# Performance work log

Hardware: AMD Instinct MI355X
Metric: run time of the kernel (lower is better)

## Reference

```python
import jax, jax.numpy as jnp
import numpy as np

L, T, D = 3, 65536, 256


def setup_inputs() -> dict:
    key = jax.random.key(0)
    ks = jax.random.split(key, 10)
    stdv = 1.0 / np.sqrt(D)
    u = lambda k, shape: jax.random.uniform(k, shape, jnp.float32, -stdv, stdv)
    return {
        "story": jax.random.normal(ks[0], (T, D), jnp.float32),
        "question": jax.random.normal(ks[1], (D,), jnp.float32),
        "Wz_f": u(ks[2], (L, D, D)),
        "bz_f": u(ks[3], (L, D)),
        "Wh_f": u(ks[4], (L, 2 * D, D)),
        "bh_f": u(ks[5], (L, D)),
        "Wz_b": u(ks[6], (L, D, D)),
        "bz_b": u(ks[7], (L, D)),
        "Wh_b": u(ks[8], (L, 2 * D, D)),
        "bh_b": u(ks[9], (L, D)),
    }


def _qrn_dir(x, q, Wz, bz, Wh, bh):
    """One QRN layer in one direction. x, q: [T, D]. Returns h states [T, D]."""
    z = jax.nn.sigmoid((x * q) @ Wz + bz)                      # [T, D]
    h_tilde = jnp.tanh(jnp.concatenate([x, q], axis=-1) @ Wh + bh)  # [T, D]
    a = 1.0 - z            # multiplicative factor on h_prev
    b = z * h_tilde        # additive term
    # linear recurrence h_t = a_t * h_{t-1} + b_t, h_0 = 0 -> associative scan
    def comb(c1, c2):
        a1, b1 = c1
        a2, b2 = c2
        return a1 * a2, a2 * b1 + b2
    _, h = jax.lax.associative_scan(comb, (a, b), axis=0)
    return h  # h[t] = hidden state after statement t


def reference(story, question, Wz_f, bz_f, Wh_f, bh_f, Wz_b, bz_b, Wh_b, bh_b):
    q = jnp.broadcast_to(question, story.shape)  # layer-0 question per step
    for layer in range(L):
        h_fwd = _qrn_dir(story, q, Wz_f[layer], bz_f[layer], Wh_f[layer], bh_f[layer])
        # backward direction: reversed story with correspondingly reversed questions
        h_bwd_rev = _qrn_dir(story[::-1], q[::-1], Wz_b[layer], bz_b[layer],
                             Wh_b[layer], bh_b[layer])
        if layer < L - 1:
            # q_{t}^{k+1} = h_fwd_t + h_bwd_t (aligned back to forward order)
            q = h_fwd + h_bwd_rev[::-1]
    return h_fwd[-1]  # final forward hidden state of last layer, [D]
```

## Files before the change

kernel.cpp:

```cpp
#include <hip/hip_runtime.h>
#include <hip/hip_bf16.h>
#include <math.h>

#define D    256
#define BT   128
#define GN   128
#define BN   64
#define NSEG 32

typedef unsigned short u16;
typedef unsigned int   u32;
typedef __attribute__((ext_vector_type(8))) short short8;
typedef __attribute__((ext_vector_type(4))) float floatx4;

__device__ __forceinline__ float b2f(u16 v) {
    union { unsigned u; float f; } x; x.u = ((unsigned)v) << 16; return x.f;
}
__device__ __forceinline__ u16 f2b(float f) {
    union { unsigned u; float f; } x; x.f = f;
    unsigned lsb = (x.u >> 16) & 1;
    x.u += 0x7fffu + lsb;
    return (u16)(x.u >> 16);
}
__device__ __forceinline__ float sigm(float x) {
    return __builtin_amdgcn_rcpf(1.0f + __expf(-x));
}
__device__ __forceinline__ float tanhfast(float x) {
    return 1.0f - 2.0f * __builtin_amdgcn_rcpf(__expf(2.0f * x) + 1.0f);
}
__device__ __forceinline__ void async16(const u16* g, u16* l) {
    __builtin_amdgcn_global_load_lds(
        (const __attribute__((address_space(1))) unsigned int*)g,
        (__attribute__((address_space(3))) unsigned int*)l, 16, 0, 0);
}

__global__ __launch_bounds__(256) void wtrans_kernel(
    const float* __restrict__ Wz_f, const float* __restrict__ Wh_f,
    const float* __restrict__ Wz_b, const float* __restrict__ Wh_b,
    u16* __restrict__ wt)
{
    int id = blockIdx.x * 256 + threadIdx.x;
    int combo = id / (3 * 65536);
    int rem   = id % (3 * 65536);
    int m = rem >> 16;
    int e = rem & 65535;
    int k = e >> 8, n = e & 255;
    int l   = combo < 3 ? combo : combo - 3;
    int dir = combo < 3 ? 0 : 1;
    float v;
    if (m == 0) {
        const float* Wz = dir ? Wz_b : Wz_f;
        v = Wz[((size_t)l * D + k) * D + n];
    } else {
        const float* Wh = dir ? Wh_b : Wh_f;
        int kk = (m == 2) ? (k + D) : k;
        v = Wh[((size_t)l * 2 * D + kk) * D + n];
    }
    wt[(size_t)combo * 3 * 65536 + (size_t)m * 65536 + (size_t)n * D + k] = f2b(v);
}

__global__ __launch_bounds__(256) void prep0_kernel(
    const float* __restrict__ story, const float* __restrict__ question,
    u16* __restrict__ xb, u16* __restrict__ q, u16* __restrict__ xq)
{
    long id = (long)blockIdx.x * 256 + threadIdx.x;
    long row = id >> 5;
    int  d0  = (int)(id & 31) * 8;
    const float* xp = story + row * D + d0;
    float4 xa = *(const float4*)xp;
    float4 xc = *(const float4*)(xp + 4);
    float xv[8] = {xa.x, xa.y, xa.z, xa.w, xc.x, xc.y, xc.z, xc.w};
    short8 xs, qs, xqs;
    #pragma unroll
    for (int i = 0; i < 8; ++i) {
        u16 qb = f2b(question[d0 + i]);
        xs[i]  = (short)f2b(xv[i]);
        qs[i]  = (short)qb;
        xqs[i] = (short)f2b(xv[i] * b2f(qb));
    }
    long o = id * 8;
    *(short8*)(xb + o) = xs;
    *(short8*)(q  + o) = qs;
    *(short8*)(xq + o) = xqs;
}

struct StageS {
    u16 ax [BT * 32]; u16 aq [BT * 32]; u16 axq[BT * 32];
    u16 bz_[GN * 32]; u16 bx_[GN * 32]; u16 bq_[GN * 32];
};
struct EpiP { float segA[NSEG][GN]; float segB[NSEG][GN]; };
union __align__(16) SharedP { StageS st; EpiP ep; };

__device__ __forceinline__ void gemm_body(
    SharedP& sh, int tid, int c, int n0,
    const u16* xbg, const u16* qg, const u16* xqg, const u16* wt,
    const float* bz, const float* bh,
    float* aggA, float* aggB, u32* abg, int FWD)
{
    const int t0   = c * BT;
    const int lane = tid & 63, w = tid >> 6;
    const int wr = w & 1, wc = w >> 1;
    const int lr   = lane & 15, quad = lane >> 4;

    const int swA   = (quad ^ ((lr >> 1) & 3)) * 8;
    const int offA0 = (wr * 64 + lr) * 32 + swA;
    const int offB0 = (wc * 32 + lr) * 32 + swA;

    floatx4 accz[4][2], acch[4][2];
    #pragma unroll
    for (int rt = 0; rt < 4; ++rt)
        #pragma unroll
        for (int ct = 0; ct < 2; ++ct) {
            accz[rt][ct] = (floatx4){0.f,0.f,0.f,0.f};
            acch[rt][ct] = (floatx4){0.f,0.f,0.f,0.f};
        }

    const int lb = (tid & ~63) * 8;

    const int arow = tid >> 2;
    const int agg_ = (tid & 3) ^ ((arow >> 1) & 3);
    const size_t goA = (size_t)(t0 + arow) * D + agg_ * 8;
    const size_t goB = (size_t)(n0 + arow) * D + agg_ * 8;
    const u16* pax  = xbg + goA;
    const u16* paq  = qg  + goA;
    const u16* paxq = xqg + goA;
    const u16* pbz  = wt + goB;
    const u16* pbx  = wt + 65536  + goB;
    const u16* pbq  = wt + 131072 + goB;

    #pragma unroll
    for (int k0 = 0; k0 < D; k0 += 32) {
        async16(pax  + k0, sh.st.ax  + lb);
        async16(paq  + k0, sh.st.aq  + lb);
        async16(paxq + k0, sh.st.axq + lb);
        async16(pbz  + k0, sh.st.bz_ + lb);
        async16(pbx  + k0, sh.st.bx_ + lb);
        async16(pbq  + k0, sh.st.bq_ + lb);
        __syncthreads();

        short8 vz[2], vx[2], vq[2];
        #pragma unroll
        for (int ct = 0; ct < 2; ++ct) {
            vz[ct] = *(const short8*)(sh.st.bz_ + offB0 + ct * 512);
            vx[ct] = *(const short8*)(sh.st.bx_ + offB0 + ct * 512);
            vq[ct] = *(const short8*)(sh.st.bq_ + offB0 + ct * 512);
        }
        #pragma unroll
        for (int rt = 0; rt < 4; ++rt) {
            short8 fxq = *(const short8*)(sh.st.axq + offA0 + rt * 512);
            short8 fx  = *(const short8*)(sh.st.ax  + offA0 + rt * 512);
            short8 fq  = *(const short8*)(sh.st.aq  + offA0 + rt * 512);
            #pragma unroll
            for (int ct = 0; ct < 2; ++ct) {
                accz[rt][ct] = __builtin_amdgcn_mfma_f32_16x16x32_bf16(fxq, vz[ct], accz[rt][ct], 0, 0, 0);
                acch[rt][ct] = __builtin_amdgcn_mfma_f32_16x16x32_bf16(fx , vx[ct], acch[rt][ct], 0, 0, 0);
                acch[rt][ct] = __builtin_amdgcn_mfma_f32_16x16x32_bf16(fq , vq[ct], acch[rt][ct], 0, 0, 0);
            }
        }
        __syncthreads();
    }

    float bzn[2], bhn[2];
    #pragma unroll
    for (int ct = 0; ct < 2; ++ct) {
        int n = n0 + wc * 32 + ct * 16 + lr;
        bzn[ct] = bz[n]; bhn[ct] = bh[n];
    }
    #pragma unroll
    for (int rt = 0; rt < 4; ++rt) {
        #pragma unroll
        for (int ct = 0; ct < 2; ++ct) {
            float av[4], bvv[4];
            #pragma unroll
            for (int r = 0; r < 4; ++r) {
                float z  = sigm(accz[rt][ct][r] + bzn[ct]);
                float ht = tanhfast(acch[rt][ct][r] + bhn[ct]);
                av[r]  = 1.0f - z;
                bvv[r] = z * ht;
            }
            float A = 1.f, B = 0.f;
            if (FWD) {
                #pragma unroll
                for (int r = 0; r < 4; ++r) { A = av[r] * A; B = fmaf(av[r], B, bvv[r]); }
            } else {
                #pragma unroll
                for (int r = 3; r >= 0; --r) { A = av[r] * A; B = fmaf(av[r], B, bvv[r]); }
            }
            int seg = wr * 16 + rt * 4 + quad;
            int col = wc * 32 + ct * 16 + lr;
            sh.ep.segA[seg][col] = A;
            sh.ep.segB[seg][col] = B;
            if (abg) {
                size_t base = (size_t)(t0 + wr * 64 + rt * 16 + quad * 4) * D + n0 + col;
                #pragma unroll
                for (int r = 0; r < 4; ++r) {
                    u32 pv = (u32)f2b(av[r]) | ((u32)f2b(bvv[r]) << 16);
                    abg[base + (size_t)r * D] = pv;
                }
            }
        }
    }
    __syncthreads();

    if (tid < GN) {
        float A = 1.f, B = 0.f;
        if (FWD) {
            #pragma unroll
            for (int sg = 0; sg < NSEG; ++sg) {
                float a = sh.ep.segA[sg][tid];
                A = a * A; B = fmaf(a, B, sh.ep.segB[sg][tid]);
            }
        } else {
            #pragma unroll
            for (int sg = NSEG - 1; sg >= 0; --sg) {
                float a = sh.ep.segA[sg][tid];
                A = a * A; B = fmaf(a, B, sh.ep.segB[sg][tid]);
            }
        }
        aggA[(size_t)c * D + n0 + tid] = A;
        aggB[(size_t)c * D + n0 + tid] = B;
    }
}

template<int FWD, int ABOUT>
__global__ __launch_bounds__(512, 4) void qrn_g5(
    const u16* __restrict__ xbg, const u16* __restrict__ qg,
    const u16* __restrict__ xqg, const u16* __restrict__ wt,
    const float* __restrict__ bz, const float* __restrict__ bh,
    float* __restrict__ aggA, float* __restrict__ aggB,
    u32* __restrict__ abg)
{
    __shared__ SharedP sh;
    const int tid  = threadIdx.x;
    const int bid  = (int)blockIdx.x;
    const int gidx = (bid & 7) * 128 + (bid >> 3);
    gemm_body(sh, tid, gidx >> 1, (gidx & 1) * GN,
              xbg, qg, xqg, wt, bz, bh, aggA, aggB, ABOUT ? abg : nullptr, FWD);
}

__global__ __launch_bounds__(512, 4) void qrn_gboth(
    const u16* __restrict__ xbg, const u16* __restrict__ qg,
    const u16* __restrict__ xqg,
    const u16* __restrict__ wtF, const u16* __restrict__ wtB,
    const float* __restrict__ bzf, const float* __restrict__ bhf,
    const float* __restrict__ bzb, const float* __restrict__ bhb,
    float* __restrict__ aggAf, float* __restrict__ aggBf,
    float* __restrict__ aggAb, float* __restrict__ aggBb,
    u32* __restrict__ abf, u32* __restrict__ abb)
{
    __shared__ SharedP sh;
    const int tid  = threadIdx.x;
    const int half = (int)blockIdx.x >> 10;
    const int bid  = (int)blockIdx.x & 1023;
    const int gidx = (bid & 7) * 128 + (bid >> 3);
    gemm_body(sh, tid, gidx >> 1, (gidx & 1) * GN,
              xbg, qg, xqg,
              half ? wtB : wtF,
              half ? bzb : bzf, half ? bhb : bhf,
              half ? aggAb : aggAf, half ? aggBb : aggBf,
              half ? abb : abf, half ? 0 : 1);
}

__global__ __launch_bounds__(256) void replay_fb(
    const u32* __restrict__ abf, const u32* __restrict__ abb,
    const float* __restrict__ hinif, const float* __restrict__ hinib,
    const u16* __restrict__ xb, u16* __restrict__ qout, u16* __restrict__ xq)
{
    __shared__ u32   sab[BT * BN];
    __shared__ u16   hf16[BT * BN];
    __shared__ float sA[4][BN], sB[4][BN], hs[4][BN];
    const int tid = threadIdx.x;
    const int c   = (int)(blockIdx.x >> 2);
    const int n0  = ((int)blockIdx.x & 3) * BN;
    const int t0  = c * BT;
    const int sg = tid >> 6, n = tid & 63;

    #pragma unroll
    for (int i = 0; i < 8; ++i) {
        int idx = i * 256 + tid;
        int row = idx >> 4, g = idx & 15;
        *(uint4*)(sab + row * BN + g * 4) =
            *(const uint4*)(abf + (size_t)(t0 + row) * D + n0 + g * 4);
    }
    __syncthreads();
    {
        float A = 1.f, B = 0.f;
        #pragma unroll
        for (int i = 0; i < 32; ++i) {
            u32 v = sab[(sg * 32 + i) * BN + n];
            float a = b2f((u16)(v & 0xffff)), b = b2f((u16)(v >> 16));
            A = a * A; B = fmaf(a, B, b);
        }
        sA[sg][n] = A; sB[sg][n] = B;
    }
    __syncthreads();
    if (tid < BN) {
        float h = hinif[(size_t)c * D + n0 + tid];
        #pragma unroll
        for (int s = 0; s < 4; ++s) {
            hs[s][tid] = h;
            h = fmaf(sA[s][tid], h, sB[s][tid]);
        }
    }
    __syncthreads();
    {
        float h = hs[sg][n];
        #pragma unroll
        for (int i = 0; i < 32; ++i) {
            int t = sg * 32 + i;
            u32 v = sab[t * BN + n];
            float a = b2f((u16)(v & 0xffff)), b = b2f((u16)(v >> 16));
            h = fmaf(a, h, b);
            hf16[t * BN + n] = f2b(h);
        }
    }
    __syncthreads();

    #pragma unroll
    for (int i = 0; i < 8; ++i) {
        int idx = i * 256 + tid;
        int row = idx >> 4, g = idx & 15;
        *(uint4*)(sab + row * BN + g * 4) =
            *(const uint4*)(abb + (size_t)(t0 + row) * D + n0 + g * 4);
    }
    __syncthreads();
    {
        float A = 1.f, B = 0.f;
        #pragma unroll
        for (int i = 31; i >= 0; --i) {
            u32 v = sab[(sg * 32 + i) * BN + n];
            float a = b2f((u16)(v & 0xffff)), b = b2f((u16)(v >> 16));
            A = a * A; B = fmaf(a, B, b);
        }
        sA[sg][n] = A; sB[sg][n] = B;
    }
    __syncthreads();
    if (tid < BN) {
        float h = hinib[(size_t)c * D + n0 + tid];
        for (int s = 3; s >= 0; --s) {
            hs[s][tid] = h;
            h = fmaf(sA[s][tid], h, sB[s][tid]);
        }
    }
    __syncthreads();
    {
        float h = hs[sg][n];
        #pragma unroll
        for (int i = 31; i >= 0; --i) {
            int t = sg * 32 + i;
            u32 v = sab[t * BN + n];
            float a = b2f((u16)(v & 0xffff)), b = b2f((u16)(v >> 16));
            h = fmaf(a, h, b);
            size_t o = (size_t)(t0 + t) * D + n0 + n;
            float qn = b2f(hf16[t * BN + n]) + h;
            u16 qb = f2b(qn);
            qout[o] = qb;
            xq[o]   = f2b(b2f(xb[o]) * b2f(qb));
        }
    }
}

__global__ __launch_bounds__(256) void replay_f(
    const u32* __restrict__ abg, const float* __restrict__ hini,
    u16* __restrict__ qout)
{
    __shared__ u32   sab[BT * BN];
    __shared__ float sA[4][BN], sB[4][BN], hs[4][BN];
    const int tid = threadIdx.x;
    const int c   = (int)(blockIdx.x >> 2);
    const int n0  = ((int)blockIdx.x & 3) * BN;
    const int t0  = c * BT;

    #pragma unroll
    for (int i = 0; i < 8; ++i) {
        int idx = i * 256 + tid;
        int row = idx >> 4, g = idx & 15;
        *(uint4*)(sab + row * BN + g * 4) =
            *(const uint4*)(abg + (size_t)(t0 + row) * D + n0 + g * 4);
    }
    __syncthreads();

    const int sg = tid >> 6, n = tid & 63;
    float A = 1.f, B = 0.f;
    #pragma unroll
    for (int i = 0; i < 32; ++i) {
        u32 v = sab[(sg * 32 + i) * BN + n];
        float a = b2f((u16)(v & 0xffff)), b = b2f((u16)(v >> 16));
        A = a * A; B = fmaf(a, B, b);
    }
    sA[sg][n] = A; sB[sg][n] = B;
    __syncthreads();
    if (tid < BN) {
        float h = hini[(size_t)c * D + n0 + tid];
        #pragma unroll
        for (int s = 0; s < 4; ++s) {
            hs[s][tid] = h;
            h = fmaf(sA[s][tid], h, sB[s][tid]);
        }
    }
    __syncthreads();
    float h = hs[sg][n];
    #pragma unroll
    for (int i = 0; i < 32; ++i) {
        int t = sg * 32 + i;
        u32 v = sab[t * BN + n];
        float a = b2f((u16)(v & 0xffff)), b = b2f((u16)(v >> 16));
        h = fmaf(a, h, b);
        qout[(size_t)(t0 + t) * D + n0 + n] = f2b(h);
    }
}

__global__ __launch_bounds__(256) void replay_b(
    const u32* __restrict__ abg, const float* __restrict__ hini,
    const u16* __restrict__ xb, u16* __restrict__ qout, u16* __restrict__ xq)
{
    __shared__ u32   sab[BT * BN];
    __shared__ float sA[4][BN], sB[4][BN], hs[4][BN];
    const int tid = threadIdx.x;
    const int c   = (int)(blockIdx.x >> 2);
    const int n0  = ((int)blockIdx.x & 3) * BN;
    const int t0  = c * BT;

    #pragma unroll
    for (int i = 0; i < 8; ++i) {
        int idx = i * 256 + tid;
        int row = idx >> 4, g = idx & 15;
        *(uint4*)(sab + row * BN + g * 4) =
            *(const uint4*)(abg + (size_t)(t0 + row) * D + n0 + g * 4);
    }
    __syncthreads();

    const int sg = tid >> 6, n = tid & 63;
    float A = 1.f, B = 0.f;
    #pragma unroll
    for (int i = 31; i >= 0; --i) {
        u32 v = sab[(sg * 32 + i) * BN + n];
        float a = b2f((u16)(v & 0xffff)), b = b2f((u16)(v >> 16));
        A = a * A; B = fmaf(a, B, b);
    }
    sA[sg][n] = A; sB[sg][n] = B;
    __syncthreads();
    if (tid < BN) {
        float h = hini[(size_t)c * D + n0 + tid];
        for (int s = 3; s >= 0; --s) {
            hs[s][tid] = h;
            h = fmaf(sA[s][tid], h, sB[s][tid]);
        }
    }
    __syncthreads();
    float h = hs[sg][n];
    #pragma unroll
    for (int i = 31; i >= 0; --i) {
        int t = sg * 32 + i;
        u32 v = sab[t * BN + n];
        float a = b2f((u16)(v & 0xffff)), b = b2f((u16)(v >> 16));
        h = fmaf(a, h, b);
        size_t o = (size_t)(t0 + t) * D + n0 + n;
        float qn = b2f(qout[o]) + h;
        u16 qb = f2b(qn);
        qout[o] = qb;
        xq[o]   = f2b(b2f(xb[o]) * b2f(qb));
    }
}

__device__ __forceinline__ void scan_body(
    const float* aggA, const float* aggB, float* hinit, float* out_final,
    int fwd, int nch, int n, int tid)
{
    __shared__ float sA[256], sB[256];
    const int per = nch >> 8;
    float lA[4], lB[4];
    float A = 1.f, B = 0.f;
    for (int j = 0; j < per; ++j) {
        int pidx = tid * per + j;
        int c = fwd ? pidx : (nch - 1 - pidx);
        float a = aggA[(size_t)c * D + n];
        float b = aggB[(size_t)c * D + n];
        lA[j] = a; lB[j] = b;
        A = a * A;
        B = fmaf(a, B, b);
    }
    sA[tid] = A; sB[tid] = B;
    __syncthreads();
    for (int off = 1; off < 256; off <<= 1) {
        float pA = 1.f, pB = 0.f;
        if (tid >= off) { pA = sA[tid - off]; pB = sB[tid - off]; }
        __syncthreads();
        if (tid >= off) {
            float cA = sA[tid], cB = sB[tid];
            sA[tid] = pA * cA;
            sB[tid] = fmaf(cA, pB, cB);
        }
        __syncthreads();
    }
    float eB = (tid > 0) ? sB[tid - 1] : 0.f;
    for (int j = 0; j < per; ++j) {
        int pidx = tid * per + j;
        int c = fwd ? pidx : (nch - 1 - pidx);
        hinit[(size_t)c * D + n] = eB;
        eB = fmaf(lA[j], eB, lB[j]);
    }
    if (out_final != nullptr && tid == 0) out_final[n] = sB[255];
}

__global__ __launch_bounds__(256) void scan_p2_kernel(
    const float* __restrict__ aggA, const float* __restrict__ aggB,
    float* __restrict__ hinit, float* __restrict__ out_final, int fwd, int nch)
{
    scan_body(aggA, aggB, hinit, out_final, fwd, nch, blockIdx.x, threadIdx.x);
}

__global__ __launch_bounds__(256) void scan_dual_kernel(
    const float* __restrict__ aggAf, const float* __restrict__ aggBf, float* __restrict__ hf,
    const float* __restrict__ aggAb, const float* __restrict__ aggBb, float* __restrict__ hb,
    int nch)
{
    int b = blockIdx.x;
    int fwd = (b < D) ? 1 : 0;
    int n = fwd ? b : (b - D);
    scan_body(fwd ? aggAf : aggAb, fwd ? aggBf : aggBb,
              fwd ? hf : hb, nullptr, fwd, nch, n, threadIdx.x);
}

extern "C" void kernel_launch(void* const* d_in, const int* in_sizes, int n_in,
                              void* d_out, int out_size, void* d_ws, size_t ws_size,
                              hipStream_t stream) {
    const float* story    = (const float*)d_in[0];
    const float* question = (const float*)d_in[1];
    const float* Wz_f = (const float*)d_in[2];
    const float* bz_f = (const float*)d_in[3];
    const float* Wh_f = (const float*)d_in[4];
    const float* bh_f = (const float*)d_in[5];
    const float* Wz_b = (const float*)d_in[6];
    const float* bz_b = (const float*)d_in[7];
    const float* Wh_b = (const float*)d_in[8];
    const float* bh_b = (const float*)d_in[9];

    const int T    = in_sizes[0] / D;
    const int NCH  = T / BT;
    const size_t TD = (size_t)T * D;
    const size_t WTE = 5 * 3 * 65536;

    const size_t needF = 3 * TD * 2 + WTE * 2 + 2 * TD * 4
                       + (size_t)4 * NCH * D * 4 + 4096;
    const bool planF = ws_size >= needF;

    dim3 blk(256);
    dim3 gblk(512);
    dim3 gGrid((unsigned)(NCH * 2));
    dim3 g2Grid((unsigned)(NCH * 4));
    dim3 rGrid((unsigned)(NCH * 4));
    dim3 pGrid((unsigned)(TD / 8 / 256));

    if (planF) {
        u16* xb = (u16*)d_ws;
        u16* q  = xb + TD;
        u16* xq = q  + TD;
        u16* wt = xq + TD;
        u32* abf = (u32*)(wt + WTE);
        u32* abb = abf + TD;
        float* aggAf = (float*)(abb + TD);
        float* aggBf = aggAf + (size_t)NCH * D;
        float* aggAb = aggBf + (size_t)NCH * D;
        float* aggBb = aggAb + (size_t)NCH * D;
        float* hinif = aggBf;
        float* hinib = aggBb;

        wtrans_kernel<<<dim3(5 * 3 * 65536 / 256), blk, 0, stream>>>(
            Wz_f, Wh_f, Wz_b, Wh_b, wt);
        prep0_kernel<<<pGrid, blk, 0, stream>>>(story, question, xb, q, xq);

        for (int l = 0; l < 3; ++l) {
            const u16*   wtf = wt + (size_t)l * 3 * 65536;
            const float* bzf = bz_f + (size_t)l * D;
            const float* bhf = bh_f + (size_t)l * D;

            if (l == 2) {
                qrn_g5<1,0><<<gGrid, gblk, 0, stream>>>(
                    xb, q, xq, wtf, bzf, bhf, aggAf, aggBf, nullptr);
                scan_p2_kernel<<<dim3(D), blk, 0, stream>>>(
                    aggAf, aggBf, hinif, (float*)d_out, 1, NCH);
                break;
            }
            const u16*   wtb = wt + (size_t)(3 + l) * 3 * 65536;
            const float* bzb = bz_b + (size_t)l * D;
            const float* bhb = bh_b + (size_t)l * D;

            qrn_gboth<<<g2Grid, gblk, 0, stream>>>(
                xb, q, xq, wtf, wtb, bzf, bhf, bzb, bhb,
                aggAf, aggBf, aggAb, aggBb, abf, abb);
            scan_dual_kernel<<<dim3(2 * D), blk, 0, stream>>>(
                aggAf, aggBf, hinif, aggAb, aggBb, hinib, NCH);
            replay_fb<<<rGrid, blk, 0, stream>>>(
                abf, abb, hinif, hinib, xb, q, xq);
        }
    } else {
        u16* xb = (u16*)d_ws;
        u16* qA = xb + TD;
        u16* qB = qA + TD;
        u16* xq = qB + TD;
        u16* wt = xq + TD;
        u32*   ab   = (u32*)(wt + WTE);
        float* aggA = (float*)(ab + TD);
        float* aggB = aggA + (size_t)NCH * D;
        float* hini = aggB;

        wtrans_kernel<<<dim3(5 * 3 * 65536 / 256), blk, 0, stream>>>(
            Wz_f, Wh_f, Wz_b, Wh_b, wt);
        prep0_kernel<<<pGrid, blk, 0, stream>>>(story, question, xb, qA, xq);

        const u16* qcur  = qA;
        u16*       qnext = qB;

        for (int l = 0; l < 3; ++l) {
            const u16*   wtf = wt + (size_t)l * 3 * 65536;
            const float* bzf = bz_f + (size_t)l * D;
            const float* bhf = bh_f + (size_t)l * D;

            if (l == 2) {
                qrn_g5<1,0><<<gGrid, gblk, 0, stream>>>(
                    xb, qcur, xq, wtf, bzf, bhf, aggA, aggB, nullptr);
                scan_p2_kernel<<<dim3(D), blk, 0, stream>>>(
                    aggA, aggB, hini, (float*)d_out, 1, NCH);
                break;
            }
            const u16*   wtb = wt + (size_t)(3 + l) * 3 * 65536;
            const float* bzb = bz_b + (size_t)l * D;
            const float* bhb = bh_b + (size_t)l * D;

            qrn_g5<1,1><<<gGrid, gblk, 0, stream>>>(
                xb, qcur, xq, wtf, bzf, bhf, aggA, aggB, ab);
            scan_p2_kernel<<<dim3(D), blk, 0, stream>>>(aggA, aggB, hini, nullptr, 1, NCH);
            replay_f<<<rGrid, blk, 0, stream>>>(ab, hini, qnext);

            qrn_g5<0,1><<<gGrid, gblk, 0, stream>>>(
                xb, qcur, xq, wtb, bzb, bhb, aggA, aggB, ab);
            scan_p2_kernel<<<dim3(D), blk, 0, stream>>>(aggA, aggB, hini, nullptr, 0, NCH);
            replay_b<<<rGrid, blk, 0, stream>>>(ab, hini, xb, qnext, xq);

            const u16* ts = qcur; qcur = qnext; qnext = (u16*)ts;
        }
    }
}
```

Before: 433.4 us.

## Double-buffer A tiles in LDS and load weight fragments directly to registers

```diff
diff --git a/kernel.cpp b/kernel.cpp
--- a/kernel.cpp
+++ b/kernel.cpp
@@ -84,10 +84,10 @@
     *(short8*)(xq + o) = xqs;
 }
 
-struct StageS {
+struct StageA {
     u16 ax [BT * 32]; u16 aq [BT * 32]; u16 axq[BT * 32];
-    u16 bz_[GN * 32]; u16 bx_[GN * 32]; u16 bq_[GN * 32];
 };
+struct StageS { StageA buf[2]; };
 struct EpiP { float segA[NSEG][GN]; float segB[NSEG][GN]; };
 union __align__(16) SharedP { StageS st; EpiP ep; };
 
@@ -104,7 +104,8 @@
 
     const int swA   = (quad ^ ((lr >> 1) & 3)) * 8;
     const int offA0 = (wr * 64 + lr) * 32 + swA;
-    const int offB0 = (wc * 32 + lr) * 32 + swA;
+
+    const u16* bp = wt + (size_t)(n0 + wc * 32 + lr) * D + quad * 8;
 
     floatx4 accz[4][2], acch[4][2];
     #pragma unroll
@@ -120,43 +121,50 @@
     const int arow = tid >> 2;
     const int agg_ = (tid & 3) ^ ((arow >> 1) & 3);
     const size_t goA = (size_t)(t0 + arow) * D + agg_ * 8;
-    const size_t goB = (size_t)(n0 + arow) * D + agg_ * 8;
     const u16* pax  = xbg + goA;
     const u16* paq  = qg  + goA;
     const u16* paxq = xqg + goA;
-    const u16* pbz  = wt + goB;
-    const u16* pbx  = wt + 65536  + goB;
-    const u16* pbq  = wt + 131072 + goB;
-
-    #pragma unroll
-    for (int k0 = 0; k0 < D; k0 += 32) {
-        async16(pax  + k0, sh.st.ax  + lb);
-        async16(paq  + k0, sh.st.aq  + lb);
-        async16(paxq + k0, sh.st.axq + lb);
-        async16(pbz  + k0, sh.st.bz_ + lb);
-        async16(pbx  + k0, sh.st.bx_ + lb);
-        async16(pbq  + k0, sh.st.bq_ + lb);
-        __syncthreads();
-
-        short8 vz[2], vx[2], vq[2];
+
+    auto stage = [&](StageA& b, int k0) {
+        async16(pax  + k0, b.ax  + lb);
+        async16(paq  + k0, b.aq  + lb);
+        async16(paxq + k0, b.axq + lb);
+    };
+
+    short8 Bz[2], Bx[2], Bq[2];
+    auto loadB = [&](int k0) {
         #pragma unroll
         for (int ct = 0; ct < 2; ++ct) {
-            vz[ct] = *(const short8*)(sh.st.bz_ + offB0 + ct * 512);
-            vx[ct] = *(const short8*)(sh.st.bx_ + offB0 + ct * 512);
-            vq[ct] = *(const short8*)(sh.st.bq_ + offB0 + ct * 512);
-        }
+            const u16* p = bp + ct * (16 * D) + k0;
+            Bz[ct] = *(const short8*)(p);
+            Bx[ct] = *(const short8*)(p + 65536);
+            Bq[ct] = *(const short8*)(p + 131072);
+        }
+    };
+
+    stage(sh.st.buf[0], 0);
+    loadB(0);
+    __syncthreads();
+
+    #pragma unroll
+    for (int kk = 0; kk < 8; ++kk) {
+        const int cur = kk & 1;
+        if (kk < 7) stage(sh.st.buf[cur ^ 1], (kk + 1) * 32);
+
+        const StageA& A = sh.st.buf[cur];
         #pragma unroll
         for (int rt = 0; rt < 4; ++rt) {
-            short8 fxq = *(const short8*)(sh.st.axq + offA0 + rt * 512);
-            short8 fx  = *(const short8*)(sh.st.ax  + offA0 + rt * 512);
-            short8 fq  = *(const short8*)(sh.st.aq  + offA0 + rt * 512);
+            short8 fxq = *(const short8*)(A.axq + offA0 + rt * 512);
+            short8 fx  = *(const short8*)(A.ax  + offA0 + rt * 512);
+            short8 fq  = *(const short8*)(A.aq  + offA0 + rt * 512);
             #pragma unroll
             for (int ct = 0; ct < 2; ++ct) {
-                accz[rt][ct] = __builtin_amdgcn_mfma_f32_16x16x32_bf16(fxq, vz[ct], accz[rt][ct], 0, 0, 0);
-                acch[rt][ct] = __builtin_amdgcn_mfma_f32_16x16x32_bf16(fx , vx[ct], acch[rt][ct], 0, 0, 0);
-                acch[rt][ct] = __builtin_amdgcn_mfma_f32_16x16x32_bf16(fq , vq[ct], acch[rt][ct], 0, 0, 0);
-            }
-        }
+                accz[rt][ct] = __builtin_amdgcn_mfma_f32_16x16x32_bf16(fxq, Bz[ct], accz[rt][ct], 0, 0, 0);
+                acch[rt][ct] = __builtin_amdgcn_mfma_f32_16x16x32_bf16(fx , Bx[ct], acch[rt][ct], 0, 0, 0);
+                acch[rt][ct] = __builtin_amdgcn_mfma_f32_16x16x32_bf16(fq , Bq[ct], acch[rt][ct], 0, 0, 0);
+            }
+        }
+        if (kk < 7) loadB((kk + 1) * 32);
         __syncthreads();
     }
 
```

Result: slower. 537.5 us (+24.0%).

## Store chunk-local prefix scan products so replay becomes elementwise

Applied to the files above, without the earlier changes.

```diff
diff --git a/kernel.cpp b/kernel.cpp
--- a/kernel.cpp
+++ b/kernel.cpp
@@ -5,7 +5,6 @@
 #define D    256
 #define BT   128
 #define GN   128
-#define BN   64
 #define NSEG 32
 
 typedef unsigned short u16;
@@ -166,38 +165,30 @@
         int n = n0 + wc * 32 + ct * 16 + lr;
         bzn[ct] = bz[n]; bhn[ct] = bh[n];
     }
+    float av[4][2][4], bvv[4][2][4];
     #pragma unroll
     for (int rt = 0; rt < 4; ++rt) {
         #pragma unroll
         for (int ct = 0; ct < 2; ++ct) {
-            float av[4], bvv[4];
             #pragma unroll
             for (int r = 0; r < 4; ++r) {
                 float z  = sigm(accz[rt][ct][r] + bzn[ct]);
                 float ht = tanhfast(acch[rt][ct][r] + bhn[ct]);
-                av[r]  = 1.0f - z;
-                bvv[r] = z * ht;
+                av[rt][ct][r]  = 1.0f - z;
+                bvv[rt][ct][r] = z * ht;
             }
             float A = 1.f, B = 0.f;
             if (FWD) {
                 #pragma unroll
-                for (int r = 0; r < 4; ++r) { A = av[r] * A; B = fmaf(av[r], B, bvv[r]); }
+                for (int r = 0; r < 4; ++r) { A = av[rt][ct][r] * A; B = fmaf(av[rt][ct][r], B, bvv[rt][ct][r]); }
             } else {
                 #pragma unroll
-                for (int r = 3; r >= 0; --r) { A = av[r] * A; B = fmaf(av[r], B, bvv[r]); }
+                for (int r = 3; r >= 0; --r) { A = av[rt][ct][r] * A; B = fmaf(av[rt][ct][r], B, bvv[rt][ct][r]); }
             }
             int seg = wr * 16 + rt * 4 + quad;
             int col = wc * 32 + ct * 16 + lr;
             sh.ep.segA[seg][col] = A;
             sh.ep.segB[seg][col] = B;
-            if (abg) {
-                size_t base = (size_t)(t0 + wr * 64 + rt * 16 + quad * 4) * D + n0 + col;
-                #pragma unroll
-                for (int r = 0; r < 4; ++r) {
-                    u32 pv = (u32)f2b(av[r]) | ((u32)f2b(bvv[r]) << 16);
-                    abg[base + (size_t)r * D] = pv;
-                }
-            }
         }
     }
     __syncthreads();
@@ -207,18 +198,50 @@
         if (FWD) {
             #pragma unroll
             for (int sg = 0; sg < NSEG; ++sg) {
-                float a = sh.ep.segA[sg][tid];
-                A = a * A; B = fmaf(a, B, sh.ep.segB[sg][tid]);
+                float a = sh.ep.segA[sg][tid], b = sh.ep.segB[sg][tid];
+                sh.ep.segA[sg][tid] = A; sh.ep.segB[sg][tid] = B;
+                A = a * A; B = fmaf(a, B, b);
             }
         } else {
             #pragma unroll
             for (int sg = NSEG - 1; sg >= 0; --sg) {
-                float a = sh.ep.segA[sg][tid];
-                A = a * A; B = fmaf(a, B, sh.ep.segB[sg][tid]);
+                float a = sh.ep.segA[sg][tid], b = sh.ep.segB[sg][tid];
+                sh.ep.segA[sg][tid] = A; sh.ep.segB[sg][tid] = B;
+                A = a * A; B = fmaf(a, B, b);
             }
         }
         aggA[(size_t)c * D + n0 + tid] = A;
         aggB[(size_t)c * D + n0 + tid] = B;
+    }
+
+    if (abg) {
+        __syncthreads();
+        #pragma unroll
+        for (int rt = 0; rt < 4; ++rt) {
+            #pragma unroll
+            for (int ct = 0; ct < 2; ++ct) {
+                int seg = wr * 16 + rt * 4 + quad;
+                int col = wc * 32 + ct * 16 + lr;
+                float Pa = sh.ep.segA[seg][col];
+                float Pb = sh.ep.segB[seg][col];
+                size_t base = (size_t)(t0 + wr * 64 + rt * 16 + quad * 4) * D + n0 + col;
+                if (FWD) {
+                    #pragma unroll
+                    for (int r = 0; r < 4; ++r) {
+                        Pa = av[rt][ct][r] * Pa;
+                        Pb = fmaf(av[rt][ct][r], Pb, bvv[rt][ct][r]);
+                        abg[base + (size_t)r * D] = (u32)f2b(Pa) | ((u32)f2b(Pb) << 16);
+                    }
+                } else {
+                    #pragma unroll
+                    for (int r = 3; r >= 0; --r) {
+                        Pa = av[rt][ct][r] * Pa;
+                        Pb = fmaf(av[rt][ct][r], Pb, bvv[rt][ct][r]);
+                        abg[base + (size_t)r * D] = (u32)f2b(Pa) | ((u32)f2b(Pb) << 16);
+                    }
+                }
+            }
+        }
     }
 }
 
@@ -261,205 +284,104 @@
               half ? abb : abf, half ? 0 : 1);
 }
 
-__global__ __launch_bounds__(256) void replay_fb(
+__global__ __launch_bounds__(256) void replay2_fb(
     const u32* __restrict__ abf, const u32* __restrict__ abb,
     const float* __restrict__ hinif, const float* __restrict__ hinib,
-    const u16* __restrict__ xb, u16* __restrict__ qout, u16* __restrict__ xq)
-{
-    __shared__ u32   sab[BT * BN];
-    __shared__ u16   hf16[BT * BN];
-    __shared__ float sA[4][BN], sB[4][BN], hs[4][BN];
-    const int tid = threadIdx.x;
-    const int c   = (int)(blockIdx.x >> 2);
-    const int n0  = ((int)blockIdx.x & 3) * BN;
-    const int t0  = c * BT;
-    const int sg = tid >> 6, n = tid & 63;
-
-    #pragma unroll
-    for (int i = 0; i < 8; ++i) {
-        int idx = i * 256 + tid;
-        int row = idx >> 4, g = idx & 15;
-        *(uint4*)(sab + row * BN + g * 4) =
-            *(const uint4*)(abf + (size_t)(t0 + row) * D + n0 + g * 4);
-    }
-    __syncthreads();
-    {
-        float A = 1.f, B = 0.f;
-        #pragma unroll
-        for (int i = 0; i < 32; ++i) {
-            u32 v = sab[(sg * 32 + i) * BN + n];
-            float a = b2f((u16)(v & 0xffff)), b = b2f((u16)(v >> 16));
-            A = a * A; B = fmaf(a, B, b);
-        }
-        sA[sg][n] = A; sB[sg][n] = B;
-    }
-    __syncthreads();
-    if (tid < BN) {
-        float h = hinif[(size_t)c * D + n0 + tid];
-        #pragma unroll
-        for (int s = 0; s < 4; ++s) {
-            hs[s][tid] = h;
-            h = fmaf(sA[s][tid], h, sB[s][tid]);
-        }
-    }
-    __syncthreads();
-    {
-        float h = hs[sg][n];
-        #pragma unroll
-        for (int i = 0; i < 32; ++i) {
-            int t = sg * 32 + i;
-            u32 v = sab[t * BN + n];
-            float a = b2f((u16)(v & 0xffff)), b = b2f((u16)(v >> 16));
-            h = fmaf(a, h, b);
-            hf16[t * BN + n] = f2b(h);
-        }
-    }
-    __syncthreads();
-
-    #pragma unroll
-    for (int i = 0; i < 8; ++i) {
-        int idx = i * 256 + tid;
-        int row = idx >> 4, g = idx & 15;
-        *(uint4*)(sab + row * BN + g * 4) =
-            *(const uint4*)(abb + (size_t)(t0 + row) * D + n0 + g * 4);
-    }
-    __syncthreads();
-    {
-        float A = 1.f, B = 0.f;
-        #pragma unroll
-        for (int i = 31; i >= 0; --i) {
-            u32 v = sab[(sg * 32 + i) * BN + n];
-            float a = b2f((u16)(v & 0xffff)), b = b2f((u16)(v >> 16));
-            A = a * A; B = fmaf(a, B, b);
-        }
-        sA[sg][n] = A; sB[sg][n] = B;
-    }
-    __syncthreads();
-    if (tid < BN) {
-        float h = hinib[(size_t)c * D + n0 + tid];
-        for (int s = 3; s >= 0; --s) {
-            hs[s][tid] = h;
-            h = fmaf(sA[s][tid], h, sB[s][tid]);
-        }
-    }
-    __syncthreads();
-    {
-        float h = hs[sg][n];
-        #pragma unroll
-        for (int i = 31; i >= 0; --i) {
-            int t = sg * 32 + i;
-            u32 v = sab[t * BN + n];
-            float a = b2f((u16)(v & 0xffff)), b = b2f((u16)(v >> 16));
-            h = fmaf(a, h, b);
-            size_t o = (size_t)(t0 + t) * D + n0 + n;
-            float qn = b2f(hf16[t * BN + n]) + h;
+    const u16* __restrict__ xb, u16* __restrict__ qout, u16* __restrict__ xq,
+    int total8)
+{
+    for (int id = (int)blockIdx.x * 256 + (int)threadIdx.x; id < total8;
+         id += (int)gridDim.x * 256) {
+        int t  = id >> 5;
+        int n0 = (id & 31) * 8;
+        int c  = t >> 7;
+        size_t o  = (size_t)t * D + n0;
+        size_t hc = (size_t)c * D + n0;
+        uint4 f0 = *(const uint4*)(abf + o);
+        uint4 f1 = *(const uint4*)(abf + o + 4);
+        uint4 g0 = *(const uint4*)(abb + o);
+        uint4 g1 = *(const uint4*)(abb + o + 4);
+        float4 hf0 = *(const float4*)(hinif + hc);
+        float4 hf1 = *(const float4*)(hinif + hc + 4);
+        float4 hb0 = *(const float4*)(hinib + hc);
+        float4 hb1 = *(const float4*)(hinib + hc + 4);
+        short8 xv = *(const short8*)(xb + o);
+        u32 fa[8] = {f0.x, f0.y, f0.z, f0.w, f1.x, f1.y, f1.z, f1.w};
+        u32 ga[8] = {g0.x, g0.y, g0.z, g0.w, g1.x, g1.y, g1.z, g1.w};
+        float hfv[8] = {hf0.x, hf0.y, hf0.z, hf0.w, hf1.x, hf1.y, hf1.z, hf1.w};
+        float hbv[8] = {hb0.x, hb0.y, hb0.z, hb0.w, hb1.x, hb1.y, hb1.z, hb1.w};
+        short8 qs, xqs;
+        #pragma unroll
+        for (int i = 0; i < 8; ++i) {
+            float hF = fmaf(b2f((u16)(fa[i] & 0xffff)), hfv[i], b2f((u16)(fa[i] >> 16)));
+            float hB = fmaf(b2f((u16)(ga[i] & 0xffff)), hbv[i], b2f((u16)(ga[i] >> 16)));
+            u16 qb = f2b(hF + hB);
+            qs[i]  = (short)qb;
+            xqs[i] = (short)f2b(b2f((u16)xv[i]) * b2f(qb));
+        }
+        *(short8*)(qout + o) = qs;
+        *(short8*)(xq + o)   = xqs;
+    }
+}
+
+__global__ __launch_bounds__(256) void replay2_f(
+    const u32* __restrict__ abg, const float* __restrict__ hini,
+    u16* __restrict__ qout, int total8)
+{
+    for (int id = (int)blockIdx.x * 256 + (int)threadIdx.x; id < total8;
+         id += (int)gridDim.x * 256) {
+        int t  = id >> 5;
+        int n0 = (id & 31) * 8;
+        int c  = t >> 7;
+        size_t o  = (size_t)t * D + n0;
+        size_t hc = (size_t)c * D + n0;
+        uint4 f0 = *(const uint4*)(abg + o);
+        uint4 f1 = *(const uint4*)(abg + o + 4);
+        float4 hf0 = *(const float4*)(hini + hc);
+        float4 hf1 = *(const float4*)(hini + hc + 4);
+        u32 fa[8] = {f0.x, f0.y, f0.z, f0.w, f1.x, f1.y, f1.z, f1.w};
+        float hfv[8] = {hf0.x, hf0.y, hf0.z, hf0.w, hf1.x, hf1.y, hf1.z, hf1.w};
+        short8 qs;
+        #pragma unroll
+        for (int i = 0; i < 8; ++i) {
+            float hF = fmaf(b2f((u16)(fa[i] & 0xffff)), hfv[i], b2f((u16)(fa[i] >> 16)));
+            qs[i] = (short)f2b(hF);
+        }
+        *(short8*)(qout + o) = qs;
+    }
+}
+
+__global__ __launch_bounds__(256) void replay2_b(
+    const u32* __restrict__ abg, const float* __restrict__ hini,
+    const u16* __restrict__ xb, u16* __restrict__ qout, u16* __restrict__ xq,
+    int total8)
+{
+    for (int id = (int)blockIdx.x * 256 + (int)threadIdx.x; id < total8;
+         id += (int)gridDim.x * 256) {
+        int t  = id >> 5;
+        int n0 = (id & 31) * 8;
+        int c  = t >> 7;
+        size_t o  = (size_t)t * D + n0;
+        size_t hc = (size_t)c * D + n0;
+        uint4 g0 = *(const uint4*)(abg + o);
+        uint4 g1 = *(const uint4*)(abg + o + 4);
+        float4 hb0 = *(const float4*)(hini + hc);
+        float4 hb1 = *(const float4*)(hini + hc + 4);
+        short8 qold = *(const short8*)(qout + o);
+        short8 xv   = *(const short8*)(xb + o);
+        u32 ga[8] = {g0.x, g0.y, g0.z, g0.w, g1.x, g1.y, g1.z, g1.w};
+        float hbv[8] = {hb0.x, hb0.y, hb0.z, hb0.w, hb1.x, hb1.y, hb1.z, hb1.w};
+        short8 qs, xqs;
+        #pragma unroll
+        for (int i = 0; i < 8; ++i) {
+            float hB = fmaf(b2f((u16)(ga[i] & 0xffff)), hbv[i], b2f((u16)(ga[i] >> 16)));
+            float qn = b2f((u16)qold[i]) + hB;
             u16 qb = f2b(qn);
-            qout[o] = qb;
-            xq[o]   = f2b(b2f(xb[o]) * b2f(qb));
-        }
-    }
-}
-
-__global__ __launch_bounds__(256) void replay_f(
-    const u32* __restrict__ abg, const float* __restrict__ hini,
-    u16* __restrict__ qout)
-{
-    __shared__ u32   sab[BT * BN];
-    __shared__ float sA[4][BN], sB[4][BN], hs[4][BN];
-    const int tid = threadIdx.x;
-    const int c   = (int)(blockIdx.x >> 2);
-    const int n0  = ((int)blockIdx.x & 3) * BN;
-    const int t0  = c * BT;
-
-    #pragma unroll
-    for (int i = 0; i < 8; ++i) {
-        int idx = i * 256 + tid;
-        int row = idx >> 4, g = idx & 15;
-        *(uint4*)(sab + row * BN + g * 4) =
-            *(const uint4*)(abg + (size_t)(t0 + row) * D + n0 + g * 4);
-    }
-    __syncthreads();
-
-    const int sg = tid >> 6, n = tid & 63;
-    float A = 1.f, B = 0.f;
-    #pragma unroll
-    for (int i = 0; i < 32; ++i) {
-        u32 v = sab[(sg * 32 + i) * BN + n];
-        float a = b2f((u16)(v & 0xffff)), b = b2f((u16)(v >> 16));
-        A = a * A; B = fmaf(a, B, b);
-    }
-    sA[sg][n] = A; sB[sg][n] = B;
-    __syncthreads();
-    if (tid < BN) {
-        float h = hini[(size_t)c * D + n0 + tid];
-        #pragma unroll
-        for (int s = 0; s < 4; ++s) {
-            hs[s][tid] = h;
-            h = fmaf(sA[s][tid], h, sB[s][tid]);
-        }
-    }
-    __syncthreads();
-    float h = hs[sg][n];
-    #pragma unroll
-    for (int i = 0; i < 32; ++i) {
-        int t = sg * 32 + i;
-        u32 v = sab[t * BN + n];
-        float a = b2f((u16)(v & 0xffff)), b = b2f((u16)(v >> 16));
-        h = fmaf(a, h, b);
-        qout[(size_t)(t0 + t) * D + n0 + n] = f2b(h);
-    }
-}
-
-__global__ __launch_bounds__(256) void replay_b(
-    const u32* __restrict__ abg, const float* __restrict__ hini,
-    const u16* __restrict__ xb, u16* __restrict__ qout, u16* __restrict__ xq)
-{
-    __shared__ u32   sab[BT * BN];
-    __shared__ float sA[4][BN], sB[4][BN], hs[4][BN];
-    const int tid = threadIdx.x;
-    const int c   = (int)(blockIdx.x >> 2);
-    const int n0  = ((int)blockIdx.x & 3) * BN;
-    const int t0  = c * BT;
-
-    #pragma unroll
-    for (int i = 0; i < 8; ++i) {
-        int idx = i * 256 + tid;
-        int row = idx >> 4, g = idx & 15;
-        *(uint4*)(sab + row * BN + g * 4) =
-            *(const uint4*)(abg + (size_t)(t0 + row) * D + n0 + g * 4);
-    }
-    __syncthreads();
-
-    const int sg = tid >> 6, n = tid & 63;
-    float A = 1.f, B = 0.f;
-    #pragma unroll
-    for (int i = 31; i >= 0; --i) {
-        u32 v = sab[(sg * 32 + i) * BN + n];
-        float a = b2f((u16)(v & 0xffff)), b = b2f((u16)(v >> 16));
-        A = a * A; B = fmaf(a, B, b);
-    }
-    sA[sg][n] = A; sB[sg][n] = B;
-    __syncthreads();
-    if (tid < BN) {
-        float h = hini[(size_t)c * D + n0 + tid];
-        for (int s = 3; s >= 0; --s) {
-            hs[s][tid] = h;
-            h = fmaf(sA[s][tid], h, sB[s][tid]);
-        }
-    }
-    __syncthreads();
-    float h = hs[sg][n];
-    #pragma unroll
-    for (int i = 31; i >= 0; --i) {
-        int t = sg * 32 + i;
-        u32 v = sab[t * BN + n];
-        float a = b2f((u16)(v & 0xffff)), b = b2f((u16)(v >> 16));
-        h = fmaf(a, h, b);
-        size_t o = (size_t)(t0 + t) * D + n0 + n;
-        float qn = b2f(qout[o]) + h;
-        u16 qb = f2b(qn);
-        qout[o] = qb;
-        xq[o]   = f2b(b2f(xb[o]) * b2f(qb));
+            qs[i]  = (short)qb;
+            xqs[i] = (short)f2b(b2f((u16)xv[i]) * b2f(qb));
+        }
+        *(short8*)(qout + o) = qs;
+        *(short8*)(xq + o)   = xqs;
     }
 }
 
@@ -540,6 +462,7 @@
     const int NCH  = T / BT;
     const size_t TD = (size_t)T * D;
     const size_t WTE = 5 * 3 * 65536;
+    const int total8 = T * 32;
 
     const size_t needF = 3 * TD * 2 + WTE * 2 + 2 * TD * 4
                        + (size_t)4 * NCH * D * 4 + 4096;
@@ -549,7 +472,7 @@
     dim3 gblk(512);
     dim3 gGrid((unsigned)(NCH * 2));
     dim3 g2Grid((unsigned)(NCH * 4));
-    dim3 rGrid((unsigned)(NCH * 4));
+    dim3 rGrid(2048);
     dim3 pGrid((unsigned)(TD / 8 / 256));
 
     if (planF) {
@@ -591,8 +514,8 @@
                 aggAf, aggBf, aggAb, aggBb, abf, abb);
             scan_dual_kernel<<<dim3(2 * D), blk, 0, stream>>>(
                 aggAf, aggBf, hinif, aggAb, aggBb, hinib, NCH);
-            replay_fb<<<rGrid, blk, 0, stream>>>(
-                abf, abb, hinif, hinib, xb, q, xq);
+            replay2_fb<<<rGrid, blk, 0, stream>>>(
+                abf, abb, hinif, hinib, xb, q, xq, total8);
         }
     } else {
         u16* xb = (u16*)d_ws;
@@ -631,12 +554,12 @@
             qrn_g5<1,1><<<gGrid, gblk, 0, stream>>>(
                 xb, qcur, xq, wtf, bzf, bhf, aggA, aggB, ab);
             scan_p2_kernel<<<dim3(D), blk, 0, stream>>>(aggA, aggB, hini, nullptr, 1, NCH);
-            replay_f<<<rGrid, blk, 0, stream>>>(ab, hini, qnext);
+            replay2_f<<<rGrid, blk, 0, stream>>>(ab, hini, qnext, total8);
 
             qrn_g5<0,1><<<gGrid, gblk, 0, stream>>>(
                 xb, qcur, xq, wtb, bzb, bhb, aggA, aggB, ab);
             scan_p2_kernel<<<dim3(D), blk, 0, stream>>>(aggA, aggB, hini, nullptr, 0, NCH);
-            replay_b<<<rGrid, blk, 0, stream>>>(ab, hini, xb, qnext, xq);
+            replay2_b<<<rGrid, blk, 0, stream>>>(ab, hini, xb, qnext, xq, total8);
 
             const u16* ts = qcur; qcur = qnext; qnext = (u16*)ts;
         }
```

After: 438.3 us. About the same (+1.1%).
